# Kernel optimization log

Hardware: AMD Instinct MI355X
Metric: run time of the kernel (lower is better)

The kernel has to match this reference:

```python
import jax, jax.numpy as jnp
import numpy as np

N = 100_000   # nodes
E = 1_600_000 # edges (avg degree 16)
D = 128       # feature dim (input = hidden = output = mlp hidden)
L = 3         # GIN layers
EPS = 0.0     # init_eps, not learned


def setup_inputs() -> dict:
    key = jax.random.key(0)
    ks = jax.random.split(key, 7)
    feat = jax.random.normal(ks[0], (N, D), jnp.float32)
    # scale weights ~ 1/sqrt(fan_in) for numerically sane activations
    W1 = jax.random.normal(ks[1], (L, D, D), jnp.float32) / np.float32(np.sqrt(D))
    b1 = jax.random.normal(ks[2], (L, D), jnp.float32) * 0.01
    W2 = jax.random.normal(ks[3], (L, D, D), jnp.float32) / np.float32(np.sqrt(D))
    b2 = jax.random.normal(ks[4], (L, D), jnp.float32) * 0.01
    src = jax.random.randint(ks[5], (E,), 0, N, dtype=jnp.int32)
    dst = jax.random.randint(ks[6], (E,), 0, N, dtype=jnp.int32)
    return {"feat": feat, "W1": W1, "b1": b1, "W2": W2, "b2": b2,
            "src": src, "dst": dst}


def reference(feat, W1, b1, W2, b2, src, dst):
    h = feat
    for i in range(L):
        # sum-aggregate neighbor (source) features into destination nodes
        neigh = jax.ops.segment_sum(h[src], dst, num_segments=N)  # [N, D]
        rst = (1.0 + EPS) * h + neigh
        # 2-layer MLP: hidden layer uses act+norm(none), last layer is plain linear
        if i < L - 1:
            h1 = jax.nn.relu(rst @ W1[i] + b1[i])
            h2 = h1 @ W2[i] + b2[i]
            h = jax.nn.relu(h2)  # ApplyNodeFunc: norm(none) -> relu
        else:
            # last GIN layer: activation 'none' everywhere
            h1 = rst @ W1[i] + b1[i]
            h = h1 @ W2[i] + b2[i]
    return h
```

## Files before the change

### kernel.cpp

```cpp
#include <hip/hip_runtime.h>
#include <hip/hip_bf16.h>

#define D 128
#define NBUCK_SHIFT 9
#define PAD_SLACK 2048

typedef __bf16 bf16x8 __attribute__((ext_vector_type(8)));
typedef float f32x4 __attribute__((ext_vector_type(4)));
typedef float f32x2 __attribute__((ext_vector_type(2)));
typedef unsigned int u32x4 __attribute__((ext_vector_type(4)));
typedef unsigned short u16x4_t __attribute__((ext_vector_type(4)));
typedef unsigned short u16x8_t __attribute__((ext_vector_type(8)));

__device__ __forceinline__ float b2f(unsigned short u) {
    unsigned int x = ((unsigned int)u) << 16;
    return __builtin_bit_cast(float, x);
}
__device__ __forceinline__ unsigned short f2b(float f) {
    __hip_bfloat16 h = __float2bfloat16(f);
    return __builtin_bit_cast(unsigned short, h);
}

__device__ __forceinline__ void acc8(f32x2* acc, u32x4 x) {
#pragma unroll
    for (int r = 0; r < 4; ++r) {
        f32x2 t;
        t[0] = __builtin_bit_cast(float, x[r] << 16);
        t[1] = __builtin_bit_cast(float, x[r] & 0xffff0000u);
        acc[r] += t;
    }
}

__global__ __launch_bounds__(256) void coarse_hist_kernel(
        const int* __restrict__ dst, int* __restrict__ bco, int E, int nbuck) {
    __shared__ int s[256];
    int t = threadIdx.x;
    s[t] = 0;
    __syncthreads();
    for (int i = blockIdx.x * 256 + t; i < E; i += gridDim.x * 256)
        atomicAdd(&s[dst[i] >> NBUCK_SHIFT], 1);
    __syncthreads();
    if (t < nbuck && s[t] > 0) atomicAdd(&bco[t], s[t]);
}

__global__ __launch_bounds__(256) void bucket_scan_kernel(
        const int* __restrict__ bco, int* __restrict__ bbase, int nbuck, int E) {
    __shared__ int s[256];
    int t = threadIdx.x;
    int c = (t < nbuck) ? bco[t] : 0;
    s[t] = c;
    __syncthreads();
    for (int o = 1; o < 256; o <<= 1) {
        int y = (t >= o) ? s[t - o] : 0;
        __syncthreads();
        s[t] += y;
        __syncthreads();
    }
    if (t < nbuck) bbase[t] = s[t] - c;
    if (t == 0) bbase[nbuck] = E;
}

__global__ __launch_bounds__(256) void bucket_kernel(
        const int* __restrict__ src, const int* __restrict__ dst,
        const int* __restrict__ bbase, int* __restrict__ bcursor,
        int2* __restrict__ pairs, int E, int nbuck) {
    __shared__ int lcnt[256];
    __shared__ int lbase[256];
    int t = threadIdx.x;
    int base = blockIdx.x * 4096;
    if (t < nbuck) lcnt[t] = 0;
    __syncthreads();
    int d[16], s[16];
#pragma unroll
    for (int k = 0; k < 16; ++k) {
        int i = base + t + k * 256;
        if (i < E) {
            d[k] = dst[i];
            s[k] = src[i];
            atomicAdd(&lcnt[d[k] >> NBUCK_SHIFT], 1);
        } else {
            d[k] = -1;
            s[k] = 0;
        }
    }
    __syncthreads();
    if (t < nbuck) {
        int c = lcnt[t];
        int g = (c > 0) ? atomicAdd(&bcursor[t], c) : 0;
        lbase[t] = bbase[t] + g;
        lcnt[t] = 0;
    }
    __syncthreads();
#pragma unroll
    for (int k = 0; k < 16; ++k) {
        if (d[k] >= 0) {
            int b = d[k] >> NBUCK_SHIFT;
            int r = atomicAdd(&lcnt[b], 1);
            pairs[lbase[b] + r] = make_int2(s[k], d[k]);
        }
    }
}

__global__ __launch_bounds__(1024) void bucket_build_kernel(
        const int2* __restrict__ pairs, const int* __restrict__ bbase,
        int2* __restrict__ rowse, int* __restrict__ col, int N, int E) {
    __shared__ int cnt[512];
    __shared__ int off[512];
    int t = threadIdx.x;
    int b = blockIdx.x;
    int s0 = bbase[b], s1 = bbase[b + 1];
    int p0 = ((s0 + 3) & ~3) + b * PAD_SLACK;
    if (t < 512) cnt[t] = 0;
    __syncthreads();
    for (int i = s0 + t; i < s1; i += 1024)
        atomicAdd(&cnt[pairs[i].y & 511], 1);
    __syncthreads();
    int c = (t < 512) ? cnt[t] : 0;
    int cp = (c + 3) & ~3;
    if (t < 512) off[t] = cp;
    __syncthreads();
    for (int o = 1; o < 512; o <<= 1) {
        int y = (t < 512 && t >= o) ? off[t - o] : 0;
        __syncthreads();
        if (t < 512) off[t] += y;
        __syncthreads();
    }
    int v0 = b << NBUCK_SHIFT;
    if (t < 512) {
        int ex = off[t] - cp;
        off[t] = ex;
        cnt[t] = 0;
        if (v0 + t < N) rowse[v0 + t] = make_int2(p0 + ex, p0 + ex + cp);
    }
    __syncthreads();
    for (int i = s0 + t; i < s1; i += 1024) {
        int2 p = pairs[i];
        int li = p.y & 511;
        int slot = p0 + off[li] + atomicAdd(&cnt[li], 1);
        col[slot] = p.x << 8;
    }
    __syncthreads();
    if (t < 512) {
        int cc = cnt[t];
        int base2 = p0 + off[t];
        int endp = base2 + ((cc + 3) & ~3);
        for (int q = base2 + cc; q < endp; ++q) col[q] = N << 8;
    }
}

__global__ void f32_to_bf16_kernel(const float4* __restrict__ in, ushort4* __restrict__ out, int n4) {
    int i = blockIdx.x * blockDim.x + threadIdx.x;
    if (i < n4) {
        float4 f = in[i];
        ushort4 o;
        o.x = f2b(f.x); o.y = f2b(f.y); o.z = f2b(f.z); o.w = f2b(f.w);
        out[i] = o;
    }
}

__global__ void wtrans_kernel(const float* __restrict__ W1, const float* __restrict__ W2,
                              unsigned short* __restrict__ W1L, unsigned short* __restrict__ W2L,
                              int total) {
    int i = blockIdx.x * blockDim.x + threadIdx.x;
    if (i < total) {
        int l = i >> 14;
        int rem = i & 16383;
        int k = rem >> 7;
        int n = rem & 127;
        int nt = n >> 4, l15 = n & 15;
        int kb = k >> 5, lg = (k >> 3) & 3, j = k & 7;
        int o = ((l * 32 + nt * 4 + kb) * 64 + lg * 16 + l15) * 8 + j;
        W1L[o] = f2b(W1[i]);
        W2L[o] = f2b(W2[i]);
    }
}

__global__ __launch_bounds__(256) void agg_kernel(
        const unsigned short* __restrict__ h, const int2* __restrict__ rowse,
        const int* __restrict__ col, unsigned short* __restrict__ rst, int N) {
    int lane = threadIdx.x & 63;
    int i = lane & 15;
    int j = lane >> 4;
    int v = blockIdx.x * 4 + (threadIdx.x >> 6);
    if (v >= N) return;

    const char* __restrict__ hb = (const char*)h;
    unsigned ioff = (unsigned)i * 16u;
    int2 se = rowse[v];
    int e = se.x + 4 * j;
    int e1 = se.y;

    f32x2 accA[4], accB[4], accC[4], accD[4];
#pragma unroll
    for (int r = 0; r < 4; ++r) {
        accA[r] = (f32x2){0.f, 0.f};
        accB[r] = (f32x2){0.f, 0.f};
        accC[r] = (f32x2){0.f, 0.f};
        accD[r] = (f32x2){0.f, 0.f};
    }

    if (j == 0) {
        u32x4 x = *(const u32x4*)(hb + (((unsigned)v << 8) + ioff));
        acc8(accA, x);
    }

    bool have = (e < e1);
    int4 c4;
    if (have) c4 = *(const int4*)(col + e);
    while (have) {
        int en = e + 16;
        bool haven = (en < e1);
        int4 c4n;
        if (haven) c4n = *(const int4*)(col + en);
        u32x4 x0 = *(const u32x4*)(hb + ((unsigned)c4.x + ioff));
        u32x4 x1 = *(const u32x4*)(hb + ((unsigned)c4.y + ioff));
        u32x4 x2 = *(const u32x4*)(hb + ((unsigned)c4.z + ioff));
        u32x4 x3 = *(const u32x4*)(hb + ((unsigned)c4.w + ioff));
        acc8(accA, x0);
        acc8(accB, x1);
        acc8(accC, x2);
        acc8(accD, x3);
        c4 = c4n;
        e = en;
        have = haven;
    }

    unsigned short outv[8];
#pragma unroll
    for (int r = 0; r < 4; ++r) {
        f32x2 s = (accA[r] + accB[r]) + (accC[r] + accD[r]);
        float lo = s[0], hi = s[1];
        lo += __shfl_xor(lo, 16);
        lo += __shfl_xor(lo, 32);
        hi += __shfl_xor(hi, 16);
        hi += __shfl_xor(hi, 32);
        outv[2 * r] = f2b(lo);
        outv[2 * r + 1] = f2b(hi);
    }
    if (j == 0) {
        u16x8_t o;
#pragma unroll
        for (int r = 0; r < 8; ++r) o[r] = outv[r];
        *(u16x8_t*)(rst + (size_t)v * D + i * 8) = o;
    }
}

__global__ __launch_bounds__(256, 4) void mlp_kernel(
        const unsigned short* __restrict__ A, const unsigned short* __restrict__ W1L,
        const unsigned short* __restrict__ W2L, const float* __restrict__ b1,
        const float* __restrict__ b2, unsigned short* __restrict__ hOut,
        float* __restrict__ fOut, int mode, int ntiles, int N) {
    __shared__ float b1s[128], b2s[128];
    __shared__ unsigned short tilebuf[4 * 2560];
    int tid = threadIdx.x;
    if (tid < 128) b1s[tid] = b1[tid];
    else b2s[tid - 128] = b2[tid - 128];
    __syncthreads();
    int wave = tid >> 6, lane = tid & 63, l15 = lane & 15, lg = lane >> 4;
    unsigned short* buf = tilebuf + wave * 2560;
    int tile = blockIdx.x * 4 + wave;
    if (tile >= ntiles) return;
    int v0 = tile << 4;

    bf16x8 bfrag[4];
    const unsigned short* arow = A + (size_t)(v0 + l15) * D + lg * 8;
#pragma unroll
    for (int kb = 0; kb < 4; ++kb) bfrag[kb] = *(const bf16x8*)(arow + kb * 32);

    f32x4 acc[8];
#pragma unroll
    for (int nt = 0; nt < 8; ++nt) acc[nt] = (f32x4){0.f, 0.f, 0.f, 0.f};
#pragma unroll
    for (int kb = 0; kb < 4; ++kb)
#pragma unroll
        for (int nt = 0; nt < 8; ++nt) {
            bf16x8 wf = *(const bf16x8*)(W1L + ((nt * 4 + kb) * 64 + lane) * 8);
            acc[nt] = __builtin_amdgcn_mfma_f32_16x16x32_bf16(wf, bfrag[kb], acc[nt], 0, 0, 0);
        }
#pragma unroll
    for (int nt = 0; nt < 8; ++nt) {
        f32x4 bias = *(const f32x4*)(b1s + nt * 16 + lg * 4);
        int kb2 = nt >> 1;
        int lgk = (nt & 1) * 2 + (lg >> 1);
        int U = kb2 * 80 + l15 * 5 + lgk;
        u16x4_t o;
#pragma unroll
        for (int r = 0; r < 4; ++r) {
            float x = acc[nt][r] + bias[r];
            if (mode == 0) x = fmaxf(x, 0.f);
            o[r] = f2b(x);
        }
        *(u16x4_t*)(buf + U * 8 + (lg & 1) * 4) = o;
    }
    bf16x8 bf2[4];
#pragma unroll
    for (int kb = 0; kb < 4; ++kb)
        bf2[kb] = *(const bf16x8*)(buf + (kb * 80 + l15 * 5 + lg) * 8);
#pragma unroll
    for (int nt = 0; nt < 8; ++nt) acc[nt] = (f32x4){0.f, 0.f, 0.f, 0.f};
#pragma unroll
    for (int kb = 0; kb < 4; ++kb)
#pragma unroll
        for (int nt = 0; nt < 8; ++nt) {
            bf16x8 wf = *(const bf16x8*)(W2L + ((nt * 4 + kb) * 64 + lane) * 8);
            acc[nt] = __builtin_amdgcn_mfma_f32_16x16x32_bf16(wf, bf2[kb], acc[nt], 0, 0, 0);
        }
    int m = v0 + l15;
    if (m < N) {
#pragma unroll
        for (int nt = 0; nt < 8; ++nt) {
            f32x4 bias = *(const f32x4*)(b2s + nt * 16 + lg * 4);
            int c0 = nt * 16 + lg * 4;
            if (mode == 0) {
                u16x4_t o;
#pragma unroll
                for (int r = 0; r < 4; ++r) o[r] = f2b(fmaxf(acc[nt][r] + bias[r], 0.f));
                *(u16x4_t*)(hOut + (size_t)m * D + c0) = o;
            } else {
                f32x4 o;
#pragma unroll
                for (int r = 0; r < 4; ++r) o[r] = acc[nt][r] + bias[r];
                *(f32x4*)(fOut + (size_t)m * D + c0) = o;
            }
        }
    }
}

extern "C" void kernel_launch(void* const* d_in, const int* in_sizes, int n_in,
                              void* d_out, int out_size, void* d_ws, size_t ws_size,
                              hipStream_t stream) {
    const float* feat = (const float*)d_in[0];
    const float* W1 = (const float*)d_in[1];
    const float* b1 = (const float*)d_in[2];
    const float* W2 = (const float*)d_in[3];
    const float* b2 = (const float*)d_in[4];
    const int* src = (const int*)d_in[5];
    const int* dst = (const int*)d_in[6];

    const int N = in_sizes[0] / D;
    const int L = in_sizes[2] / D;
    const int E = in_sizes[5];

    char* w = (char*)d_ws;
    size_t off = 0;
    auto alloc = [&](size_t bytes) {
        void* p = w + off;
        off = (off + bytes + 255) & ~(size_t)255;
        return p;
    };
    unsigned short* bufA = (unsigned short*)alloc((size_t)(N + 1) * D * 2);
    unsigned short* bufB = (unsigned short*)alloc((size_t)(N + 1) * D * 2);
    size_t unionBytes = (size_t)(N + 16) * D * 2;
    if ((size_t)E * 8 > unionBytes) unionBytes = (size_t)E * 8;
    unsigned short* bufR = (unsigned short*)alloc(unionBytes);
    int2* pairs = (int2*)bufR;
    int* col = (int*)alloc(((size_t)E + 256 * PAD_SLACK + 16) * 4);
    int2* rowse = (int2*)alloc((size_t)N * 8);
    int* bco = (int*)alloc(512 * 4);
    int* bcursor = bco + 256;
    int* bbase = (int*)alloc(257 * 4);
    unsigned short* W1L = (unsigned short*)alloc((size_t)L * 16384 * 2);
    unsigned short* W2L = (unsigned short*)alloc((size_t)L * 16384 * 2);

    int nbuck = (N + (1 << NBUCK_SHIFT) - 1) >> NBUCK_SHIFT;

    hipMemsetAsync(bco, 0, 512 * 4, stream);
    hipMemsetAsync(bufA + (size_t)N * D, 0, D * 2, stream);
    hipMemsetAsync(bufB + (size_t)N * D, 0, D * 2, stream);
    coarse_hist_kernel<<<512, 256, 0, stream>>>(dst, bco, E, nbuck);
    bucket_scan_kernel<<<1, 256, 0, stream>>>(bco, bbase, nbuck, E);
    bucket_kernel<<<(E + 4095) / 4096, 256, 0, stream>>>(src, dst, bbase, bcursor, pairs, E, nbuck);
    bucket_build_kernel<<<nbuck, 1024, 0, stream>>>(pairs, bbase, rowse, col, N, E);

    int n4 = N * D / 4;
    f32_to_bf16_kernel<<<(n4 + 255) / 256, 256, 0, stream>>>((const float4*)feat, (ushort4*)bufA, n4);
    int wtotal = L * D * D;
    wtrans_kernel<<<(wtotal + 255) / 256, 256, 0, stream>>>(W1, W2, W1L, W2L, wtotal);

    int ntiles = (N + 15) / 16;
    int aggBlocks = (N + 3) / 4;
    int mlpGrid = (ntiles + 3) / 4;
    const unsigned short* hin[3] = {bufA, bufB, bufA};
    unsigned short* hout[3] = {bufB, bufA, nullptr};
    for (int i = 0; i < L; ++i) {
        int mode = (i == L - 1) ? 1 : 0;
        agg_kernel<<<aggBlocks, 256, 0, stream>>>(hin[i], rowse, col, bufR, N);
        mlp_kernel<<<mlpGrid, 256, 0, stream>>>(bufR, W1L + (size_t)i * 16384, W2L + (size_t)i * 16384,
                                                b1 + i * D, b2 + i * D, hout[i], (float*)d_out,
                                                mode, ntiles, N);
    }
}
```

Before: 441.0 us.

## Add fixed 16-slot inline row head for neighbor lists and pack edge pairs

Each node now gets a 16-entry row head holding its own index plus up to 15 neighbors, padded with a zero row. Any remaining neighbors overflow into the CSR column array. The aggregation kernel does one unconditional batch of four gathers per lane group from the row head before looping over overflow, which removes the serial rowse-then-col dependency and the branch on the self-term. Edge pairs are packed into 32 bits (src<<9 | local dst) to halve bucket traffic, and index loads use nontemporal hints. This costs 6.4MB of extra row-head storage and wasted gathers of the zero row for low-degree nodes.

```diff
diff --git a/kernel.cpp b/kernel.cpp
--- a/kernel.cpp
+++ b/kernel.cpp
@@ -8,14 +8,12 @@
 typedef __bf16 bf16x8 __attribute__((ext_vector_type(8)));
 typedef float f32x4 __attribute__((ext_vector_type(4)));
 typedef float f32x2 __attribute__((ext_vector_type(2)));
+typedef int i32x4 __attribute__((ext_vector_type(4)));
+typedef int i32x2 __attribute__((ext_vector_type(2)));
 typedef unsigned int u32x4 __attribute__((ext_vector_type(4)));
 typedef unsigned short u16x4_t __attribute__((ext_vector_type(4)));
 typedef unsigned short u16x8_t __attribute__((ext_vector_type(8)));
 
-__device__ __forceinline__ float b2f(unsigned short u) {
-    unsigned int x = ((unsigned int)u) << 16;
-    return __builtin_bit_cast(float, x);
-}
 __device__ __forceinline__ unsigned short f2b(float f) {
     __hip_bfloat16 h = __float2bfloat16(f);
     return __builtin_bit_cast(unsigned short, h);
@@ -63,7 +61,7 @@
 __global__ __launch_bounds__(256) void bucket_kernel(
         const int* __restrict__ src, const int* __restrict__ dst,
         const int* __restrict__ bbase, int* __restrict__ bcursor,
-        int2* __restrict__ pairs, int E, int nbuck) {
+        unsigned int* __restrict__ pairs, int E, int nbuck) {
     __shared__ int lcnt[256];
     __shared__ int lbase[256];
     int t = threadIdx.x;
@@ -96,14 +94,15 @@
         if (d[k] >= 0) {
             int b = d[k] >> NBUCK_SHIFT;
             int r = atomicAdd(&lcnt[b], 1);
-            pairs[lbase[b] + r] = make_int2(s[k], d[k]);
+            pairs[lbase[b] + r] = ((unsigned)s[k] << 9) | ((unsigned)d[k] & 511u);
         }
     }
 }
 
 __global__ __launch_bounds__(1024) void bucket_build_kernel(
-        const int2* __restrict__ pairs, const int* __restrict__ bbase,
-        int2* __restrict__ rowse, int* __restrict__ col, int N, int E) {
+        const unsigned int* __restrict__ pairs, const int* __restrict__ bbase,
+        i32x2* __restrict__ rowse, int* __restrict__ col, int* __restrict__ rowhead,
+        int N, int E) {
     __shared__ int cnt[512];
     __shared__ int off[512];
     int t = threadIdx.x;
@@ -113,11 +112,11 @@
     if (t < 512) cnt[t] = 0;
     __syncthreads();
     for (int i = s0 + t; i < s1; i += 1024)
-        atomicAdd(&cnt[pairs[i].y & 511], 1);
-    __syncthreads();
-    int c = (t < 512) ? cnt[t] : 0;
-    int cp = (c + 3) & ~3;
-    if (t < 512) off[t] = cp;
+        atomicAdd(&cnt[pairs[i] & 511u], 1);
+    __syncthreads();
+    int deg = (t < 512) ? cnt[t] : 0;
+    int ovp = (deg > 15) ? ((deg - 15 + 3) & ~3) : 0;
+    if (t < 512) off[t] = ovp;
     __syncthreads();
     for (int o = 1; o < 512; o <<= 1) {
         int y = (t < 512 && t >= o) ? off[t - o] : 0;
@@ -126,25 +125,39 @@
         __syncthreads();
     }
     int v0 = b << NBUCK_SHIFT;
+    int zoff = N << 8;
     if (t < 512) {
-        int ex = off[t] - cp;
+        int ex = off[t] - ovp;
         off[t] = ex;
         cnt[t] = 0;
-        if (v0 + t < N) rowse[v0 + t] = make_int2(p0 + ex, p0 + ex + cp);
+        int v = v0 + t;
+        if (v < N) {
+            i32x2 se;
+            se[0] = p0 + ex;
+            se[1] = p0 + ex + ovp;
+            rowse[v] = se;
+            int* rhv = rowhead + (size_t)v * 16;
+            rhv[0] = v << 8;
+            int ninl = deg < 15 ? deg : 15;
+            for (int q = 1 + ninl; q < 16; ++q) rhv[q] = zoff;
+        }
     }
     __syncthreads();
     for (int i = s0 + t; i < s1; i += 1024) {
-        int2 p = pairs[i];
-        int li = p.y & 511;
-        int slot = p0 + off[li] + atomicAdd(&cnt[li], 1);
-        col[slot] = p.x << 8;
+        unsigned int p = pairs[i];
+        int li = (int)(p & 511u);
+        int x = (int)(p >> 9);
+        int s = atomicAdd(&cnt[li], 1);
+        if (s < 15) rowhead[(size_t)(v0 + li) * 16 + 1 + s] = x << 8;
+        else        col[p0 + off[li] + (s - 15)] = x << 8;
     }
     __syncthreads();
     if (t < 512) {
         int cc = cnt[t];
+        int ovreal = (cc > 15) ? cc - 15 : 0;
         int base2 = p0 + off[t];
-        int endp = base2 + ((cc + 3) & ~3);
-        for (int q = base2 + cc; q < endp; ++q) col[q] = N << 8;
+        int endp = base2 + ((ovreal + 3) & ~3);
+        for (int q = base2 + ovreal; q < endp; ++q) col[q] = zoff;
     }
 }
 
@@ -176,8 +189,9 @@
 }
 
 __global__ __launch_bounds__(256) void agg_kernel(
-        const unsigned short* __restrict__ h, const int2* __restrict__ rowse,
-        const int* __restrict__ col, unsigned short* __restrict__ rst, int N) {
+        const unsigned short* __restrict__ h, const i32x2* __restrict__ rowse,
+        const int* __restrict__ col, const i32x4* __restrict__ rowhead,
+        unsigned short* __restrict__ rst, int N) {
     int lane = threadIdx.x & 63;
     int i = lane & 15;
     int j = lane >> 4;
@@ -186,9 +200,9 @@
 
     const char* __restrict__ hb = (const char*)h;
     unsigned ioff = (unsigned)i * 16u;
-    int2 se = rowse[v];
-    int e = se.x + 4 * j;
-    int e1 = se.y;
+
+    i32x4 c4 = __builtin_nontemporal_load(&rowhead[(size_t)v * 4 + j]);
+    i32x2 se = __builtin_nontemporal_load(&rowse[v]);
 
     f32x2 accA[4], accB[4], accC[4], accD[4];
 #pragma unroll
@@ -199,28 +213,36 @@
         accD[r] = (f32x2){0.f, 0.f};
     }
 
-    if (j == 0) {
-        u32x4 x = *(const u32x4*)(hb + (((unsigned)v << 8) + ioff));
-        acc8(accA, x);
-    }
-
+    u32x4 x0 = *(const u32x4*)(hb + ((unsigned)c4[0] + ioff));
+    u32x4 x1 = *(const u32x4*)(hb + ((unsigned)c4[1] + ioff));
+    u32x4 x2 = *(const u32x4*)(hb + ((unsigned)c4[2] + ioff));
+    u32x4 x3 = *(const u32x4*)(hb + ((unsigned)c4[3] + ioff));
+
+    int e = se[0] + 4 * j;
+    int e1 = se[1];
     bool have = (e < e1);
-    int4 c4;
-    if (have) c4 = *(const int4*)(col + e);
+    i32x4 o4;
+    if (have) o4 = __builtin_nontemporal_load((const i32x4*)(col + e));
+
+    acc8(accA, x0);
+    acc8(accB, x1);
+    acc8(accC, x2);
+    acc8(accD, x3);
+
     while (have) {
         int en = e + 16;
         bool haven = (en < e1);
-        int4 c4n;
-        if (haven) c4n = *(const int4*)(col + en);
-        u32x4 x0 = *(const u32x4*)(hb + ((unsigned)c4.x + ioff));
-        u32x4 x1 = *(const u32x4*)(hb + ((unsigned)c4.y + ioff));
-        u32x4 x2 = *(const u32x4*)(hb + ((unsigned)c4.z + ioff));
-        u32x4 x3 = *(const u32x4*)(hb + ((unsigned)c4.w + ioff));
-        acc8(accA, x0);
-        acc8(accB, x1);
-        acc8(accC, x2);
-        acc8(accD, x3);
-        c4 = c4n;
+        i32x4 o4n;
+        if (haven) o4n = __builtin_nontemporal_load((const i32x4*)(col + en));
+        u32x4 y0 = *(const u32x4*)(hb + ((unsigned)o4[0] + ioff));
+        u32x4 y1 = *(const u32x4*)(hb + ((unsigned)o4[1] + ioff));
+        u32x4 y2 = *(const u32x4*)(hb + ((unsigned)o4[2] + ioff));
+        u32x4 y3 = *(const u32x4*)(hb + ((unsigned)o4[3] + ioff));
+        acc8(accA, y0);
+        acc8(accB, y1);
+        acc8(accC, y2);
+        acc8(accD, y3);
+        o4 = o4n;
         e = en;
         have = haven;
     }
@@ -351,11 +373,12 @@
     unsigned short* bufA = (unsigned short*)alloc((size_t)(N + 1) * D * 2);
     unsigned short* bufB = (unsigned short*)alloc((size_t)(N + 1) * D * 2);
     size_t unionBytes = (size_t)(N + 16) * D * 2;
-    if ((size_t)E * 8 > unionBytes) unionBytes = (size_t)E * 8;
+    if ((size_t)E * 4 > unionBytes) unionBytes = (size_t)E * 4;
     unsigned short* bufR = (unsigned short*)alloc(unionBytes);
-    int2* pairs = (int2*)bufR;
+    unsigned int* pairs = (unsigned int*)bufR;
     int* col = (int*)alloc(((size_t)E + 256 * PAD_SLACK + 16) * 4);
-    int2* rowse = (int2*)alloc((size_t)N * 8);
+    int* rowhead = (int*)alloc((size_t)N * 16 * 4);
+    i32x2* rowse = (i32x2*)alloc((size_t)N * 8);
     int* bco = (int*)alloc(512 * 4);
     int* bcursor = bco + 256;
     int* bbase = (int*)alloc(257 * 4);
@@ -370,7 +393,7 @@
     coarse_hist_kernel<<<512, 256, 0, stream>>>(dst, bco, E, nbuck);
     bucket_scan_kernel<<<1, 256, 0, stream>>>(bco, bbase, nbuck, E);
     bucket_kernel<<<(E + 4095) / 4096, 256, 0, stream>>>(src, dst, bbase, bcursor, pairs, E, nbuck);
-    bucket_build_kernel<<<nbuck, 1024, 0, stream>>>(pairs, bbase, rowse, col, N, E);
+    bucket_build_kernel<<<nbuck, 1024, 0, stream>>>(pairs, bbase, rowse, col, rowhead, N, E);
 
     int n4 = N * D / 4;
     f32_to_bf16_kernel<<<(n4 + 255) / 256, 256, 0, stream>>>((const float4*)feat, (ushort4*)bufA, n4);
@@ -384,7 +407,7 @@
     unsigned short* hout[3] = {bufB, bufA, nullptr};
     for (int i = 0; i < L; ++i) {
         int mode = (i == L - 1) ? 1 : 0;
-        agg_kernel<<<aggBlocks, 256, 0, stream>>>(hin[i], rowse, col, bufR, N);
+        agg_kernel<<<aggBlocks, 256, 0, stream>>>(hin[i], rowse, col, (const i32x4*)rowhead, bufR, N);
         mlp_kernel<<<mlpGrid, 256, 0, stream>>>(bufR, W1L + (size_t)i * 16384, W2L + (size_t)i * 16384,
                                                 b1 + i * D, b2 + i * D, hout[i], (float*)d_out,
                                                 mode, ntiles, N);
```

New measurement: 436.0 us. No clear change (-1.1%).
